# Performance work log

Hardware: AMD Instinct MI355X
Metric: run time of the kernel (lower is better)

The kernel has to match this reference:

```python
import jax, jax.numpy as jnp
import numpy as np

B, DIM, H, W = 8, 384, 64, 64
HEADS = 8
D = DIM // HEADS            # 48, per-head channel dim
DH = D // 2                 # 24
D2 = D // 3 * 2             # 32, conv_up hidden width (ratio=3)


def setup_inputs() -> dict:
    key = jax.random.key(0)
    ks = jax.random.split(key, 12)
    rn = lambda k, s, sc=0.05: jax.random.normal(k, s, dtype=jnp.float32) * sc
    return {
        "x": rn(ks[0], (B, DIM, H, W), 1.0),
        "w_qkv": rn(ks[1], (3 * DIM, DIM)),          # 1x1 conv dim->3dim, no bias
        "w_dw": rn(ks[2], (3 * DIM, 1, 3, 3)),       # depthwise 3x3, groups=3dim
        "temperature": jnp.ones((HEADS, 1, 1), jnp.float32),
        "w_ar": rn(ks[3], (1, D)),                   # conv_attn_right
        "w_vr": rn(ks[4], (DH, D)),                  # conv_v_right
        "w_up1": rn(ks[5], (D2, DH)),                # conv_up[0]
        "b_up1": jnp.zeros((D2,), jnp.float32),
        "ln_g": jnp.ones((D2, HEADS, 1), jnp.float32),   # LayerNorm([D2, 8, 1])
        "ln_b": jnp.zeros((D2, HEADS, 1), jnp.float32),
        "w_up2": rn(ks[6], (D, D2)),                 # conv_up[3]
        "b_up2": jnp.zeros((D,), jnp.float32),
        "w_al": rn(ks[7], (DH, D)),                  # conv_attn_left
        "w_vl": rn(ks[8], (DH, D)),                  # conv_v_left
        "w_proj": rn(ks[9], (DIM, HEADS)),           # project_out: Conv2d(heads, dim, 1)
    }


def reference(x, w_qkv, w_dw, temperature, w_ar, w_vr, w_up1, b_up1,
              ln_g, ln_b, w_up2, b_up2, w_al, w_vl, w_proj):
    b, c, h, w = x.shape
    hw = h * w
    # qkv = dwconv3x3(conv1x1(x)); the torch module computes this identically in
    # both spatial_pool and channel_pool, so compute once.
    qkv = jnp.einsum('oc,bchw->bohw', w_qkv, x)
    qkv = jax.lax.conv_general_dilated(
        qkv, w_dw, window_strides=(1, 1), padding='SAME',
        feature_group_count=3 * c, dimension_numbers=('NCHW', 'OIHW', 'NCHW'))
    q, k, v = jnp.split(qkv, 3, axis=1)
    hsplit = lambda t: t.reshape(b, HEADS, D, hw)        # 'b (head c) h w -> b head c (h w)'
    q, k, v = hsplit(q), hsplit(k), hsplit(v)
    l2n = lambda t: t / jnp.maximum(jnp.linalg.norm(t, axis=-1, keepdims=True), 1e-12)
    # elementwise q*k attention, temperature-scaled, softmax over spatial (hw)
    attn = jax.nn.softmax(l2n(q) * l2n(k) * temperature, axis=-1)   # [b,heads,D,hw]

    # ---- spatial_pool branch (produces channel gate) ----
    input_x = jnp.einsum('od,bhdn->bhon', w_vr, v)                  # [b,heads,DH,hw]
    cmask = jax.nn.softmax(jnp.einsum('od,bhdn->bhon', w_ar, attn), axis=-1)  # [b,heads,1,hw]
    ctx = jnp.einsum('bhin,bhjn->bhji', cmask, input_x)             # [b,heads,DH,1]
    ctx = ctx.transpose(0, 2, 1, 3)                                 # [b,DH,heads,1]
    t = jnp.einsum('op,bphl->bohl', w_up1, ctx) + b_up1[None, :, None, None]  # [b,D2,8,1]
    mu = t.mean(axis=(1, 2, 3), keepdims=True)
    var = t.var(axis=(1, 2, 3), keepdims=True)
    t = (t - mu) / jnp.sqrt(var + 1e-5) * ln_g[None] + ln_b[None]
    t = jax.nn.relu(t)
    t = jnp.einsum('op,bphl->bohl', w_up2, t) + b_up2[None, :, None, None]    # [b,D,8,1]
    # torch .view(b, head*d, 1, 1) on a [b, d, head, 1] tensor: plain reshape
    mask_ch = jax.nn.sigmoid(t).reshape(b, c, 1, 1)
    out_spatial = x * mask_ch

    # ---- channel_pool branch (produces spatial gate) ----
    g_x = jnp.einsum('od,bhdn->bhon', w_al, attn)                   # [b,heads,DH,hw]
    avg_x = jax.nn.softmax(g_x.mean(axis=-1), axis=-1)              # [b,heads,DH]
    theta_x = jnp.einsum('od,bhdn->bhon', w_vl, v)                  # [b,heads,DH,hw]
    mask_sp = jax.nn.sigmoid(jnp.einsum('bho,bhon->bhn', avg_x, theta_x))
    mask_sp = mask_sp.reshape(b, HEADS, h, w)
    mask_sp = jnp.einsum('oh,bhxy->boxy', w_proj, mask_sp)          # project_out
    out_channel = x * mask_sp

    return out_spatial + out_channel
```

## Files before the change

### kernel.cpp

```cpp
#include <hip/hip_runtime.h>
#include <math.h>
#include <stdint.h>

#define B_     8
#define DIM_   384
#define HEADS_ 8
#define D_     48
#define DH_    24
#define D2_    32
#define HW_    4096
#define IMG    64
#define CH3    1152

typedef __attribute__((ext_vector_type(8))) __bf16   bf16x8;
typedef __attribute__((ext_vector_type(4))) float    f32x4;
typedef __attribute__((ext_vector_type(8))) unsigned short u16x8;

__device__ __forceinline__ float b2f(unsigned short h){
  union { uint32_t u; float f; } v; v.u = ((uint32_t)h) << 16; return v.f;
}
__device__ __forceinline__ unsigned short f2b(float f){
  union { float f; uint32_t u; } v; v.f = f;
  uint32_t r = v.u + 0x7fffu + ((v.u >> 16) & 1u);
  return (unsigned short)(r >> 16);
}

__device__ __forceinline__ float wred_sum(float v){
#pragma unroll
  for (int m = 32; m; m >>= 1) v += __shfl_xor(v, m);
  return v;
}
__device__ __forceinline__ float wred_max(float v){
#pragma unroll
  for (int m = 32; m; m >>= 1) v = fmaxf(v, __shfl_xor(v, m));
  return v;
}
__device__ __forceinline__ float wred_min(float v){
#pragma unroll
  for (int m = 32; m; m >>= 1) v = fminf(v, __shfl_xor(v, m));
  return v;
}
template<int OP>
__device__ __forceinline__ float block_red(float v, float* lds){
  if (OP == 0) v = wred_sum(v);
  else if (OP == 1) v = wred_max(v);
  else v = wred_min(v);
  const int lane = threadIdx.x & 63;
  const int wid  = threadIdx.x >> 6;
  __syncthreads();
  if (lane == 0) lds[wid] = v;
  __syncthreads();
  const int nw = blockDim.x >> 6;
  float r = lds[0];
  for (int i = 1; i < nw; ++i){
    float o = lds[i];
    if (OP == 0) r += o; else if (OP == 1) r = fmaxf(r, o); else r = fminf(r, o);
  }
  return r;
}

__device__ __forceinline__ void dwplane16(const unsigned short* __restrict__ plane,
                                          const float* w9, int y, int x0, float* acc16){
#pragma unroll
  for (int j = 0; j < 16; ++j) acc16[j] = 0.f;
#pragma unroll
  for (int dy = -1; dy <= 1; ++dy){
    const int yy = y + dy;
    if ((unsigned)yy >= (unsigned)IMG) continue;
    const unsigned short* rp = plane + yy * IMG;
    u16x8 C0 = *reinterpret_cast<const u16x8*>(rp + x0);
    u16x8 C1 = *reinterpret_cast<const u16x8*>(rp + x0 + 8);
    float rw[18];
    rw[0]  = (x0 > 0)  ? b2f(rp[x0 - 1])  : 0.f;
    rw[17] = (x0 < 48) ? b2f(rp[x0 + 16]) : 0.f;
#pragma unroll
    for (int j = 0; j < 8; ++j){ rw[1+j] = b2f(C0[j]); rw[9+j] = b2f(C1[j]); }
    const float w0 = w9[(dy+1)*3], w1 = w9[(dy+1)*3+1], w2 = w9[(dy+1)*3+2];
#pragma unroll
    for (int j = 0; j < 16; ++j)
      acc16[j] = fmaf(rw[j], w0, fmaf(rw[j+1], w1, fmaf(rw[j+2], w2, acc16[j])));
  }
}

__global__ __launch_bounds__(256)
void k_cvtw(const float* __restrict__ w, unsigned short* __restrict__ wb){
  const int i = (blockIdx.x * 256 + threadIdx.x) * 4;
  float4 v = *reinterpret_cast<const float4*>(w + i);
  wb[i+0] = f2b(v.x); wb[i+1] = f2b(v.y); wb[i+2] = f2b(v.z); wb[i+3] = f2b(v.w);
}

__global__ __launch_bounds__(256)
void k_prep(const float* __restrict__ x, unsigned short* __restrict__ xT){
  __shared__ unsigned short Ts[64][66];
  const int t = threadIdx.x;
  const float* xb = x + ((size_t)blockIdx.z * DIM_ + blockIdx.y * 64) * HW_ + blockIdx.x * 64;
#pragma unroll
  for (int rr = 0; rr < 4; ++rr){
    const int r = (t >> 4) + rr * 16;
    const int c = (t & 15) * 4;
    float4 v = *reinterpret_cast<const float4*>(xb + (size_t)r * HW_ + c);
    Ts[r][c+0] = f2b(v.x); Ts[r][c+1] = f2b(v.y); Ts[r][c+2] = f2b(v.z); Ts[r][c+3] = f2b(v.w);
  }
  __syncthreads();
  const int rn = t >> 2, kc = (t & 3) * 16;
  unsigned short* yb = xT + ((size_t)blockIdx.z * HW_ + blockIdx.x * 64 + rn) * DIM_
                          + blockIdx.y * 64 + kc;
  u16x8 o0, o1;
#pragma unroll
  for (int j = 0; j < 8; ++j){ o0[j] = Ts[kc + j][rn]; o1[j] = Ts[kc + 8 + j][rn]; }
  *reinterpret_cast<u16x8*>(yb)     = o0;
  *reinterpret_cast<u16x8*>(yb + 8) = o1;
}

__global__ __launch_bounds__(256)
void k_gemm(const unsigned short* __restrict__ wb, const unsigned short* __restrict__ xT,
            unsigned short* __restrict__ qkv){
  const int b  = blockIdx.z;
  const int m0 = blockIdx.y * 128;
  const int n0 = blockIdx.x * 128;
  __shared__ unsigned short As[2][128 * 64];
  __shared__ unsigned short Bs[2][128 * 64];
  const int t = threadIdx.x;
  const int lane = t & 63;
  const int fr = lane & 15;
  const int ld = lane >> 4;
  const int w = t >> 6, wr = w >> 1, wc = w & 1;
  f32x4 acc[4][4];
#pragma unroll
  for (int i = 0; i < 4; ++i)
#pragma unroll
    for (int j = 0; j < 4; ++j) acc[i][j] = (f32x4){0.f,0.f,0.f,0.f};

  const unsigned short* Ag = wb + (size_t)m0 * DIM_;
  const unsigned short* Bg = xT + ((size_t)b * HW_ + n0) * DIM_;

  auto stage = [&](int buf, int k0){
#pragma unroll
    for (int i = 0; i < 4; ++i){
      const int q = i * 256 + t;
      const int qb = q & ~63;
      const int r = q >> 3, c = q & 7;
      const int cs = c ^ (r & 7);
      __builtin_amdgcn_global_load_lds(
        (const __attribute__((address_space(1))) void*)(Ag + (size_t)r * DIM_ + k0 + cs * 8),
        (__attribute__((address_space(3))) void*)(&As[buf][qb * 8]), 16, 0, 0);
    }
#pragma unroll
    for (int i = 0; i < 4; ++i){
      const int q = i * 256 + t;
      const int qb = q & ~63;
      const int r = q >> 3, c = q & 7;
      const int cs = c ^ (r & 7);
      __builtin_amdgcn_global_load_lds(
        (const __attribute__((address_space(1))) void*)(Bg + (size_t)r * DIM_ + k0 + cs * 8),
        (__attribute__((address_space(3))) void*)(&Bs[buf][qb * 8]), 16, 0, 0);
    }
  };

  stage(0, 0);
  for (int it = 0; it < 6; ++it){
    const int cur = it & 1;
    if (it < 5){
      stage(cur ^ 1, (it + 1) * 64);
      asm volatile("s_waitcnt vmcnt(8)" ::: "memory");
    } else {
      asm volatile("s_waitcnt vmcnt(0)" ::: "memory");
    }
    __builtin_amdgcn_s_barrier();
    asm volatile("" ::: "memory");
#pragma unroll
    for (int ks = 0; ks < 2; ++ks){
      bf16x8 af[4], bfr[4];
#pragma unroll
      for (int mi = 0; mi < 4; ++mi){
        const int row = wr * 64 + mi * 16 + fr;
        const int cc = (ks * 4 + ld) ^ (row & 7);
        af[mi] = *reinterpret_cast<const bf16x8*>(&As[cur][row * 64 + cc * 8]);
      }
#pragma unroll
      for (int ni = 0; ni < 4; ++ni){
        const int row = wc * 64 + ni * 16 + fr;
        const int cc = (ks * 4 + ld) ^ (row & 7);
        bfr[ni] = *reinterpret_cast<const bf16x8*>(&Bs[cur][row * 64 + cc * 8]);
      }
#pragma unroll
      for (int mi = 0; mi < 4; ++mi)
#pragma unroll
        for (int ni = 0; ni < 4; ++ni)
          acc[mi][ni] = __builtin_amdgcn_mfma_f32_16x16x32_bf16(af[mi], bfr[ni], acc[mi][ni], 0, 0, 0);
    }
    asm volatile("" ::: "memory");
    __builtin_amdgcn_s_barrier();
  }
  unsigned short* yb = qkv + ((size_t)b * CH3 + m0) * HW_ + n0;
#pragma unroll
  for (int mi = 0; mi < 4; ++mi){
    const int rbase = wr * 64 + mi * 16 + (lane >> 4) * 4;
#pragma unroll
    for (int ni = 0; ni < 4; ++ni){
      const int col = wc * 64 + ni * 16 + (lane & 15);
#pragma unroll
      for (int r = 0; r < 4; ++r)
        yb[(size_t)(rbase + r) * HW_ + col] = f2b(acc[mi][ni][r]);
    }
  }
}

__global__ __launch_bounds__(256)
void k_dwqk(unsigned short* __restrict__ qkv, const float* __restrict__ w_dw,
            const float* __restrict__ temperature, const float* __restrict__ w_ar,
            float* __restrict__ prm){
  const int pc = blockIdx.x;
  const int ch = pc % DIM_;
  const int b  = pc / DIM_;
  const int d  = ch % D_;
  const int head = ch / D_;
  unsigned short* qp = qkv + ((size_t)b * CH3 + ch) * HW_;
  unsigned short* kp = qp + (size_t)DIM_ * HW_;
  const int t  = threadIdx.x;
  const int y  = t >> 2;
  const int x0 = (t & 3) * 16;
  float wq9[9], wk9[9];
#pragma unroll
  for (int i = 0; i < 9; ++i){ wq9[i] = w_dw[ch*9+i]; wk9[i] = w_dw[(DIM_+ch)*9+i]; }
  float aq[16], ak[16];
  dwplane16(qp, wq9, y, x0, aq);
  dwplane16(kp, wk9, y, x0, ak);
  unsigned short qs[16], kss[16];
#pragma unroll
  for (int j = 0; j < 16; ++j){ qs[j] = f2b(aq[j]); kss[j] = f2b(ak[j]); }
  __shared__ float lds[8];
  float p[16];
  float sq = 0.f, sk = 0.f, pmx = -3.0e38f, pmn = 3.0e38f;
#pragma unroll
  for (int j = 0; j < 16; ++j){
    const float fq = b2f(qs[j]), fk = b2f(kss[j]);
    sq = fmaf(fq, fq, sq); sk = fmaf(fk, fk, sk);
    p[j] = fq * fk; pmx = fmaxf(pmx, p[j]); pmn = fminf(pmn, p[j]);
  }
  sq  = block_red<0>(sq, lds);
  sk  = block_red<0>(sk, lds);
  pmx = block_red<1>(pmx, lds);
  pmn = block_red<2>(pmn, lds);
  const float nq = fmaxf(sqrtf(sq), 1e-12f);
  const float nk = fmaxf(sqrtf(sk), 1e-12f);
  const float c  = temperature[head] / (nq * nk);
  const float m  = (c >= 0.f) ? c * pmx : c * pmn;
  float se = 0.f;
#pragma unroll
  for (int j = 0; j < 16; ++j) se += expf(fmaf(c, p[j], -m));
  se = block_red<0>(se, lds);
  u16x8 o0, o1;
#pragma unroll
  for (int j = 0; j < 8; ++j){ o0[j] = qs[j]; o1[j] = qs[8+j]; }
  *reinterpret_cast<u16x8*>(qp + (size_t)y * IMG + x0)     = o0;
  *reinterpret_cast<u16x8*>(qp + (size_t)y * IMG + x0 + 8) = o1;
#pragma unroll
  for (int j = 0; j < 8; ++j){ o0[j] = kss[j]; o1[j] = kss[8+j]; }
  *reinterpret_cast<u16x8*>(kp + (size_t)y * IMG + x0)     = o0;
  *reinterpret_cast<u16x8*>(kp + (size_t)y * IMG + x0 + 8) = o1;
  if (t == 0){
    prm[pc*3+0] = c;
    prm[pc*3+1] = m;
    prm[pc*3+2] = w_ar[d] / se;
  }
}

__global__ __launch_bounds__(256)
void k_dwv(unsigned short* __restrict__ qkv, const float* __restrict__ w_dw){
  const int pc = blockIdx.x;
  const int ch = pc % DIM_;
  const int b  = pc / DIM_;
  const int cv = 2*DIM_ + ch;
  unsigned short* plane = qkv + ((size_t)b * CH3 + cv) * HW_;
  const int t  = threadIdx.x;
  const int y  = t >> 2;
  const int x0 = (t & 3) * 16;
  float w9[9];
#pragma unroll
  for (int i = 0; i < 9; ++i) w9[i] = w_dw[cv*9+i];
  float acc16[16];
  dwplane16(plane, w9, y, x0, acc16);
  __syncthreads();
  u16x8 o0, o1;
#pragma unroll
  for (int j = 0; j < 8; ++j){ o0[j] = f2b(acc16[j]); o1[j] = f2b(acc16[8+j]); }
  *reinterpret_cast<u16x8*>(plane + (size_t)y * IMG + x0)     = o0;
  *reinterpret_cast<u16x8*>(plane + (size_t)y * IMG + x0 + 8) = o1;
}

__global__ __launch_bounds__(256)
void k_attn_a(const unsigned short* __restrict__ dqkv, const float* __restrict__ prm,
              float* __restrict__ abuf){
  const int bh   = blockIdx.y;
  const int head = bh & 7, b = bh >> 3;
  const int t = threadIdx.x;
  const int px0 = (blockIdx.x * 256 + t) * 2;
  __shared__ float pc[D_ * 3];
  for (int i = t; i < D_ * 3; i += 256) pc[i] = prm[bh * (D_ * 3) + i];
  __syncthreads();
  const unsigned short* qb = dqkv + ((size_t)b * CH3 + head * D_) * HW_ + px0;
  const unsigned short* kb = qb + (size_t)DIM_ * HW_;
  float a0 = 0.f, a1 = 0.f;
  for (int d = 0; d < D_; ++d){
    const uint32_t qv = *reinterpret_cast<const uint32_t*>(qb + (size_t)d * HW_);
    const uint32_t kv = *reinterpret_cast<const uint32_t*>(kb + (size_t)d * HW_);
    const float cc = pc[d*3], mm = pc[d*3+1], ww = pc[d*3+2];
    const float p0 = b2f((unsigned short)qv) * b2f((unsigned short)kv);
    const float p1 = b2f((unsigned short)(qv >> 16)) * b2f((unsigned short)(kv >> 16));
    a0 = fmaf(ww, expf(fmaf(cc, p0, -mm)), a0);
    a1 = fmaf(ww, expf(fmaf(cc, p1, -mm)), a1);
  }
  float2 o; o.x = a0; o.y = a1;
  *reinterpret_cast<float2*>(abuf + (size_t)bh * HW_ + px0) = o;
}

__global__ __launch_bounds__(256)
void k_cmask(float* __restrict__ abuf){
  const int bh = blockIdx.x;
  float* a = abuf + (size_t)bh * HW_;
  __shared__ float lds[8];
  const int t = threadIdx.x;
  float va[16];
  float mx = -3.0e38f;
#pragma unroll
  for (int i = 0; i < 16; ++i){ va[i] = a[t + i*256]; mx = fmaxf(mx, va[i]); }
  mx = block_red<1>(mx, lds);
  float s = 0.f;
#pragma unroll
  for (int i = 0; i < 16; ++i){ va[i] = expf(va[i]-mx); s += va[i]; }
  s = block_red<0>(s, lds);
  const float inv = 1.f / s;
#pragma unroll
  for (int i = 0; i < 16; ++i) a[t + i*256] = va[i]*inv;
}

__global__ __launch_bounds__(256)
void k_vctx(const unsigned short* __restrict__ dqkv, const float* __restrict__ abuf,
            float* __restrict__ vctx){
  const int bid  = blockIdx.x;
  const int d    = bid % D_;
  const int head = (bid / D_) % HEADS_;
  const int b    = bid / (D_ * HEADS_);
  const unsigned short* vp = dqkv + ((size_t)b * CH3 + 2*DIM_ + head*D_ + d) * HW_;
  const float* cm = abuf + ((size_t)(b * HEADS_ + head)) * HW_;
  __shared__ float lds[8];
  const int t = threadIdx.x;
  float s = 0.f;
  u16x8 v0 = *reinterpret_cast<const u16x8*>(vp + t * 16);
  u16x8 v1 = *reinterpret_cast<const u16x8*>(vp + t * 16 + 8);
#pragma unroll
  for (int j = 0; j < 8; ++j) s = fmaf(cm[t*16 + j],     b2f(v0[j]), s);
#pragma unroll
  for (int j = 0; j < 8; ++j) s = fmaf(cm[t*16 + 8 + j], b2f(v1[j]), s);
  s = block_red<0>(s, lds);
  if (t == 0) vctx[bid] = s;
}

__global__ __launch_bounds__(256)
void k_spmask(const unsigned short* __restrict__ dqkv, const float* __restrict__ w_al,
              const float* __restrict__ w_vl, float* __restrict__ spb){
  const int bh   = blockIdx.y;
  const int head = bh & 7, b = bh >> 3;
  const int t = threadIdx.x;
  const int px0 = (blockIdx.x * 256 + t) * 2;
  __shared__ float u[D_];
  __shared__ float avg[DH_];
  if (t < DH_){
    float s = 0.f;
    for (int d = 0; d < D_; ++d) s += w_al[t*D_ + d];
    avg[t] = s * (1.f/(float)HW_);
  }
  __syncthreads();
  if (t == 0){
    float mx = avg[0];
    for (int o = 1; o < DH_; ++o) mx = fmaxf(mx, avg[o]);
    float s = 0.f;
    for (int o = 0; o < DH_; ++o){ avg[o] = expf(avg[o]-mx); s += avg[o]; }
    const float inv = 1.f/s;
    for (int o = 0; o < DH_; ++o) avg[o] *= inv;
  }
  __syncthreads();
  if (t < D_){
    float s = 0.f;
    for (int o = 0; o < DH_; ++o) s = fmaf(avg[o], w_vl[o*D_ + t], s);
    u[t] = s;
  }
  __syncthreads();
  const unsigned short* vb = dqkv + ((size_t)b * CH3 + 2*DIM_ + head*D_) * HW_ + px0;
  float a0 = 0.f, a1 = 0.f;
  for (int d = 0; d < D_; ++d){
    const uint32_t vv = *reinterpret_cast<const uint32_t*>(vb + (size_t)d * HW_);
    const float ud = u[d];
    a0 = fmaf(ud, b2f((unsigned short)vv), a0);
    a1 = fmaf(ud, b2f((unsigned short)(vv >> 16)), a1);
  }
  float2 o;
  o.x = 1.f/(1.f + expf(-a0));
  o.y = 1.f/(1.f + expf(-a1));
  *reinterpret_cast<float2*>(spb + (size_t)bh * HW_ + px0) = o;
}

__global__ __launch_bounds__(256)
void k_maskch(const float* __restrict__ vctx, const float* __restrict__ w_vr,
              const float* __restrict__ w_up1, const float* __restrict__ b_up1,
              const float* __restrict__ ln_g, const float* __restrict__ ln_b,
              const float* __restrict__ w_up2, const float* __restrict__ b_up2,
              float* __restrict__ mch){
  const int b = blockIdx.x;
  const int t = threadIdx.x;
  __shared__ float vc[HEADS_*D_];
  __shared__ float cx[HEADS_*DH_];
  __shared__ float t1[D2_*HEADS_];
  __shared__ float lds[8];
  for (int i = t; i < HEADS_*D_; i += 256) vc[i] = vctx[b*HEADS_*D_ + i];
  __syncthreads();
  if (t < HEADS_*DH_){
    const int head = t / DH_, o = t % DH_;
    float s = 0.f;
    for (int d = 0; d < D_; ++d) s = fmaf(w_vr[o*D_+d], vc[head*D_+d], s);
    cx[head*DH_+o] = s;
  }
  __syncthreads();
  const int o2 = t >> 3, hh = t & 7;
  float val = b_up1[o2];
  for (int o = 0; o < DH_; ++o) val = fmaf(w_up1[o2*DH_+o], cx[hh*DH_+o], val);
  const float mu  = block_red<0>(val, lds) * (1.f/256.f);
  const float dv  = val - mu;
  const float var = block_red<0>(dv*dv, lds) * (1.f/256.f);
  float yv = dv / sqrtf(var + 1e-5f);
  yv = fmaf(yv, ln_g[t], ln_b[t]);
  yv = fmaxf(yv, 0.f);
  t1[t] = yv;
  __syncthreads();
  for (int idx = t; idx < D_*HEADS_; idx += 256){
    const int d = idx >> 3, head2 = idx & 7;
    float s = b_up2[d];
    for (int o = 0; o < D2_; ++o) s = fmaf(w_up2[d*D2_+o], t1[o*HEADS_+head2], s);
    mch[b*DIM_ + idx] = 1.f/(1.f + expf(-s));
  }
}

__global__ __launch_bounds__(256)
void k_out(const float* __restrict__ x, const float* __restrict__ spb,
           const float* __restrict__ mch, const float* __restrict__ w_proj,
           float* __restrict__ out){
  const int b  = blockIdx.z;
  const int c0 = blockIdx.y * 16;
  const int n  = blockIdx.x * 1024 + threadIdx.x * 4;
  float4 sv[8];
#pragma unroll
  for (int h = 0; h < 8; ++h)
    sv[h] = *reinterpret_cast<const float4*>(spb + ((size_t)(b*8+h))*HW_ + n);
  for (int ci = 0; ci < 16; ++ci){
    const int c = c0 + ci;
    const float g = mch[b*DIM_ + c];
    float4 gv; gv.x = g; gv.y = g; gv.z = g; gv.w = g;
#pragma unroll
    for (int h = 0; h < 8; ++h){
      const float wp = w_proj[c*8+h];
      gv.x = fmaf(wp, sv[h].x, gv.x); gv.y = fmaf(wp, sv[h].y, gv.y);
      gv.z = fmaf(wp, sv[h].z, gv.z); gv.w = fmaf(wp, sv[h].w, gv.w);
    }
    const size_t off = ((size_t)b*DIM_ + c)*HW_ + n;
    float4 xv = *reinterpret_cast<const float4*>(x + off);
    xv.x *= gv.x; xv.y *= gv.y; xv.z *= gv.z; xv.w *= gv.w;
    *reinterpret_cast<float4*>(out + off) = xv;
  }
}

extern "C" void kernel_launch(void* const* d_in, const int* in_sizes, int n_in,
                              void* d_out, int out_size, void* d_ws, size_t ws_size,
                              hipStream_t stream) {
  const float* x      = (const float*)d_in[0];
  const float* w_qkv  = (const float*)d_in[1];
  const float* w_dw   = (const float*)d_in[2];
  const float* temp   = (const float*)d_in[3];
  const float* w_ar   = (const float*)d_in[4];
  const float* w_vr   = (const float*)d_in[5];
  const float* w_up1  = (const float*)d_in[6];
  const float* b_up1  = (const float*)d_in[7];
  const float* ln_g   = (const float*)d_in[8];
  const float* ln_b   = (const float*)d_in[9];
  const float* w_up2  = (const float*)d_in[10];
  const float* b_up2  = (const float*)d_in[11];
  const float* w_al   = (const float*)d_in[12];
  const float* w_vl   = (const float*)d_in[13];
  const float* w_proj = (const float*)d_in[14];
  float* out = (float*)d_out;

  unsigned short* qkvb = (unsigned short*)d_ws;
  unsigned short* xT   = qkvb + (size_t)B_*CH3*HW_;
  unsigned short* wb   = xT + (size_t)B_*HW_*DIM_;
  float* prm  = (float*)(wb + (size_t)CH3*DIM_);
  float* abuf = prm + 3*B_*HEADS_*D_;
  float* vctx = abuf + (size_t)B_*HEADS_*HW_;
  float* spb  = vctx + B_*HEADS_*D_;
  float* mch  = spb + (size_t)B_*HEADS_*HW_;

  k_cvtw<<<dim3((CH3*DIM_)/1024), 256, 0, stream>>>(w_qkv, wb);
  k_prep<<<dim3(HW_/64, DIM_/64, B_), 256, 0, stream>>>(x, xT);
  k_gemm<<<dim3(HW_/128, CH3/128, B_), 256, 0, stream>>>(wb, xT, qkvb);
  k_dwqk<<<dim3(B_*DIM_), 256, 0, stream>>>(qkvb, w_dw, temp, w_ar, prm);
  k_dwv<<<dim3(B_*DIM_), 256, 0, stream>>>(qkvb, w_dw);
  k_attn_a<<<dim3(8, B_*HEADS_), 256, 0, stream>>>(qkvb, prm, abuf);
  k_cmask<<<dim3(B_*HEADS_), 256, 0, stream>>>(abuf);
  k_vctx<<<dim3(B_*HEADS_*D_), 256, 0, stream>>>(qkvb, abuf, vctx);
  k_spmask<<<dim3(8, B_*HEADS_), 256, 0, stream>>>(qkvb, w_al, w_vl, spb);
  k_maskch<<<dim3(B_), 256, 0, stream>>>(vctx, w_vr, w_up1, b_up1, ln_g, ln_b,
                                         w_up2, b_up2, mch);
  k_out<<<dim3(HW_/1024, DIM_/16, B_), 256, 0, stream>>>(x, spb, mch, w_proj, out);
}
```

Measured before the change: 262.5 us.

## Fuse prep kernels, store q*k product, fold V dwconv and softmax into consumers

```diff
diff --git a/kernel.cpp b/kernel.cpp
--- a/kernel.cpp
+++ b/kernel.cpp
@@ -15,6 +15,7 @@
 typedef __attribute__((ext_vector_type(8))) __bf16   bf16x8;
 typedef __attribute__((ext_vector_type(4))) float    f32x4;
 typedef __attribute__((ext_vector_type(8))) unsigned short u16x8;
+typedef __attribute__((ext_vector_type(4))) unsigned short u16x4;
 
 __device__ __forceinline__ float b2f(unsigned short h){
   union { uint32_t u; float f; } v; v.u = ((uint32_t)h) << 16; return v.f;
@@ -82,18 +83,44 @@
   }
 }
 
-__global__ __launch_bounds__(256)
-void k_cvtw(const float* __restrict__ w, unsigned short* __restrict__ wb){
-  const int i = (blockIdx.x * 256 + threadIdx.x) * 4;
-  float4 v = *reinterpret_cast<const float4*>(w + i);
-  wb[i+0] = f2b(v.x); wb[i+1] = f2b(v.y); wb[i+2] = f2b(v.z); wb[i+3] = f2b(v.w);
-}
-
-__global__ __launch_bounds__(256)
-void k_prep(const float* __restrict__ x, unsigned short* __restrict__ xT){
+__device__ __forceinline__ void dwplane4(const unsigned short* __restrict__ plane,
+                                         const float* w9, int y, int x0, float* acc4){
+#pragma unroll
+  for (int j = 0; j < 4; ++j) acc4[j] = 0.f;
+#pragma unroll
+  for (int dy = -1; dy <= 1; ++dy){
+    const int yy = y + dy;
+    if ((unsigned)yy >= (unsigned)IMG) continue;
+    const unsigned short* rp = plane + yy * IMG;
+    u16x4 C = *reinterpret_cast<const u16x4*>(rp + x0);
+    float rw[6];
+    rw[0] = (x0 > 0)  ? b2f(rp[x0 - 1]) : 0.f;
+    rw[5] = (x0 < 60) ? b2f(rp[x0 + 4]) : 0.f;
+#pragma unroll
+    for (int j = 0; j < 4; ++j) rw[1+j] = b2f(C[j]);
+    const float w0 = w9[(dy+1)*3], w1 = w9[(dy+1)*3+1], w2 = w9[(dy+1)*3+2];
+#pragma unroll
+    for (int j = 0; j < 4; ++j)
+      acc4[j] = fmaf(rw[j], w0, fmaf(rw[j+1], w1, fmaf(rw[j+2], w2, acc4[j])));
+  }
+}
+
+__global__ __launch_bounds__(256)
+void k_prep2(const float* __restrict__ x, const float* __restrict__ w,
+             unsigned short* __restrict__ xT, unsigned short* __restrict__ wb){
   __shared__ unsigned short Ts[64][66];
   const int t = threadIdx.x;
-  const float* xb = x + ((size_t)blockIdx.z * DIM_ + blockIdx.y * 64) * HW_ + blockIdx.x * 64;
+  if (blockIdx.x < 432){
+    const int i = (blockIdx.x * 256 + t) * 4;
+    float4 v = *reinterpret_cast<const float4*>(w + i);
+    wb[i+0] = f2b(v.x); wb[i+1] = f2b(v.y); wb[i+2] = f2b(v.z); wb[i+3] = f2b(v.w);
+    return;
+  }
+  const int id = blockIdx.x - 432;
+  const int bz = id / 384;
+  const int r2 = id % 384;
+  const int by = r2 / 64, bx = r2 % 64;
+  const float* xb = x + ((size_t)bz * DIM_ + by * 64) * HW_ + bx * 64;
 #pragma unroll
   for (int rr = 0; rr < 4; ++rr){
     const int r = (t >> 4) + rr * 16;
@@ -103,8 +130,7 @@
   }
   __syncthreads();
   const int rn = t >> 2, kc = (t & 3) * 16;
-  unsigned short* yb = xT + ((size_t)blockIdx.z * HW_ + blockIdx.x * 64 + rn) * DIM_
-                          + blockIdx.y * 64 + kc;
+  unsigned short* yb = xT + ((size_t)bz * HW_ + bx * 64 + rn) * DIM_ + by * 64 + kc;
   u16x8 o0, o1;
 #pragma unroll
   for (int j = 0; j < 8; ++j){ o0[j] = Ts[kc + j][rn]; o1[j] = Ts[kc + 8 + j][rn]; }
@@ -112,7 +138,7 @@
   *reinterpret_cast<u16x8*>(yb + 8) = o1;
 }
 
-__global__ __launch_bounds__(256)
+__global__ __launch_bounds__(512, 4)
 void k_gemm(const unsigned short* __restrict__ wb, const unsigned short* __restrict__ xT,
             unsigned short* __restrict__ qkv){
   const int b  = blockIdx.z;
@@ -124,10 +150,11 @@
   const int lane = t & 63;
   const int fr = lane & 15;
   const int ld = lane >> 4;
-  const int w = t >> 6, wr = w >> 1, wc = w & 1;
-  f32x4 acc[4][4];
-#pragma unroll
-  for (int i = 0; i < 4; ++i)
+  const int w = t >> 6;
+  const int wr = w >> 1, wc = w & 1;
+  f32x4 acc[2][4];
+#pragma unroll
+  for (int i = 0; i < 2; ++i)
 #pragma unroll
     for (int j = 0; j < 4; ++j) acc[i][j] = (f32x4){0.f,0.f,0.f,0.f};
 
@@ -136,8 +163,8 @@
 
   auto stage = [&](int buf, int k0){
 #pragma unroll
-    for (int i = 0; i < 4; ++i){
-      const int q = i * 256 + t;
+    for (int i = 0; i < 2; ++i){
+      const int q = i * 512 + t;
       const int qb = q & ~63;
       const int r = q >> 3, c = q & 7;
       const int cs = c ^ (r & 7);
@@ -146,8 +173,8 @@
         (__attribute__((address_space(3))) void*)(&As[buf][qb * 8]), 16, 0, 0);
     }
 #pragma unroll
-    for (int i = 0; i < 4; ++i){
-      const int q = i * 256 + t;
+    for (int i = 0; i < 2; ++i){
+      const int q = i * 512 + t;
       const int qb = q & ~63;
       const int r = q >> 3, c = q & 7;
       const int cs = c ^ (r & 7);
@@ -162,7 +189,7 @@
     const int cur = it & 1;
     if (it < 5){
       stage(cur ^ 1, (it + 1) * 64);
-      asm volatile("s_waitcnt vmcnt(8)" ::: "memory");
+      asm volatile("s_waitcnt vmcnt(4)" ::: "memory");
     } else {
       asm volatile("s_waitcnt vmcnt(0)" ::: "memory");
     }
@@ -170,10 +197,10 @@
     asm volatile("" ::: "memory");
 #pragma unroll
     for (int ks = 0; ks < 2; ++ks){
-      bf16x8 af[4], bfr[4];
-#pragma unroll
-      for (int mi = 0; mi < 4; ++mi){
-        const int row = wr * 64 + mi * 16 + fr;
+      bf16x8 af[2], bfr[4];
+#pragma unroll
+      for (int mi = 0; mi < 2; ++mi){
+        const int row = wr * 32 + mi * 16 + fr;
         const int cc = (ks * 4 + ld) ^ (row & 7);
         af[mi] = *reinterpret_cast<const bf16x8*>(&As[cur][row * 64 + cc * 8]);
       }
@@ -184,7 +211,7 @@
         bfr[ni] = *reinterpret_cast<const bf16x8*>(&Bs[cur][row * 64 + cc * 8]);
       }
 #pragma unroll
-      for (int mi = 0; mi < 4; ++mi)
+      for (int mi = 0; mi < 2; ++mi)
 #pragma unroll
         for (int ni = 0; ni < 4; ++ni)
           acc[mi][ni] = __builtin_amdgcn_mfma_f32_16x16x32_bf16(af[mi], bfr[ni], acc[mi][ni], 0, 0, 0);
@@ -194,8 +221,8 @@
   }
   unsigned short* yb = qkv + ((size_t)b * CH3 + m0) * HW_ + n0;
 #pragma unroll
-  for (int mi = 0; mi < 4; ++mi){
-    const int rbase = wr * 64 + mi * 16 + (lane >> 4) * 4;
+  for (int mi = 0; mi < 2; ++mi){
+    const int rbase = wr * 32 + mi * 16 + (lane >> 4) * 4;
 #pragma unroll
     for (int ni = 0; ni < 4; ++ni){
       const int col = wc * 64 + ni * 16 + (lane & 15);
@@ -216,7 +243,7 @@
   const int d  = ch % D_;
   const int head = ch / D_;
   unsigned short* qp = qkv + ((size_t)b * CH3 + ch) * HW_;
-  unsigned short* kp = qp + (size_t)DIM_ * HW_;
+  const unsigned short* kp = qp + (size_t)DIM_ * HW_;
   const int t  = threadIdx.x;
   const int y  = t >> 2;
   const int x0 = (t & 3) * 16;
@@ -226,17 +253,18 @@
   float aq[16], ak[16];
   dwplane16(qp, wq9, y, x0, aq);
   dwplane16(kp, wk9, y, x0, ak);
-  unsigned short qs[16], kss[16];
-#pragma unroll
-  for (int j = 0; j < 16; ++j){ qs[j] = f2b(aq[j]); kss[j] = f2b(ak[j]); }
   __shared__ float lds[8];
-  float p[16];
+  float pr[16];
+  unsigned short pb[16];
   float sq = 0.f, sk = 0.f, pmx = -3.0e38f, pmn = 3.0e38f;
 #pragma unroll
   for (int j = 0; j < 16; ++j){
-    const float fq = b2f(qs[j]), fk = b2f(kss[j]);
+    const float fq = b2f(f2b(aq[j]));
+    const float fk = b2f(f2b(ak[j]));
     sq = fmaf(fq, fq, sq); sk = fmaf(fk, fk, sk);
-    p[j] = fq * fk; pmx = fmaxf(pmx, p[j]); pmn = fminf(pmn, p[j]);
+    pb[j] = f2b(fq * fk);
+    pr[j] = b2f(pb[j]);
+    pmx = fmaxf(pmx, pr[j]); pmn = fminf(pmn, pr[j]);
   }
   sq  = block_red<0>(sq, lds);
   sk  = block_red<0>(sk, lds);
@@ -248,45 +276,18 @@
   const float m  = (c >= 0.f) ? c * pmx : c * pmn;
   float se = 0.f;
 #pragma unroll
-  for (int j = 0; j < 16; ++j) se += expf(fmaf(c, p[j], -m));
+  for (int j = 0; j < 16; ++j) se += expf(fmaf(c, pr[j], -m));
   se = block_red<0>(se, lds);
   u16x8 o0, o1;
 #pragma unroll
-  for (int j = 0; j < 8; ++j){ o0[j] = qs[j]; o1[j] = qs[8+j]; }
+  for (int j = 0; j < 8; ++j){ o0[j] = pb[j]; o1[j] = pb[8+j]; }
   *reinterpret_cast<u16x8*>(qp + (size_t)y * IMG + x0)     = o0;
   *reinterpret_cast<u16x8*>(qp + (size_t)y * IMG + x0 + 8) = o1;
-#pragma unroll
-  for (int j = 0; j < 8; ++j){ o0[j] = kss[j]; o1[j] = kss[8+j]; }
-  *reinterpret_cast<u16x8*>(kp + (size_t)y * IMG + x0)     = o0;
-  *reinterpret_cast<u16x8*>(kp + (size_t)y * IMG + x0 + 8) = o1;
   if (t == 0){
     prm[pc*3+0] = c;
     prm[pc*3+1] = m;
     prm[pc*3+2] = w_ar[d] / se;
   }
-}
-
-__global__ __launch_bounds__(256)
-void k_dwv(unsigned short* __restrict__ qkv, const float* __restrict__ w_dw){
-  const int pc = blockIdx.x;
-  const int ch = pc % DIM_;
-  const int b  = pc / DIM_;
-  const int cv = 2*DIM_ + ch;
-  unsigned short* plane = qkv + ((size_t)b * CH3 + cv) * HW_;
-  const int t  = threadIdx.x;
-  const int y  = t >> 2;
-  const int x0 = (t & 3) * 16;
-  float w9[9];
-#pragma unroll
-  for (int i = 0; i < 9; ++i) w9[i] = w_dw[cv*9+i];
-  float acc16[16];
-  dwplane16(plane, w9, y, x0, acc16);
-  __syncthreads();
-  u16x8 o0, o1;
-#pragma unroll
-  for (int j = 0; j < 8; ++j){ o0[j] = f2b(acc16[j]); o1[j] = f2b(acc16[8+j]); }
-  *reinterpret_cast<u16x8*>(plane + (size_t)y * IMG + x0)     = o0;
-  *reinterpret_cast<u16x8*>(plane + (size_t)y * IMG + x0 + 8) = o1;
 }
 
 __global__ __launch_bounds__(256)
@@ -299,78 +300,75 @@
   __shared__ float pc[D_ * 3];
   for (int i = t; i < D_ * 3; i += 256) pc[i] = prm[bh * (D_ * 3) + i];
   __syncthreads();
-  const unsigned short* qb = dqkv + ((size_t)b * CH3 + head * D_) * HW_ + px0;
-  const unsigned short* kb = qb + (size_t)DIM_ * HW_;
+  const unsigned short* pbase = dqkv + ((size_t)b * CH3 + head * D_) * HW_ + px0;
   float a0 = 0.f, a1 = 0.f;
   for (int d = 0; d < D_; ++d){
-    const uint32_t qv = *reinterpret_cast<const uint32_t*>(qb + (size_t)d * HW_);
-    const uint32_t kv = *reinterpret_cast<const uint32_t*>(kb + (size_t)d * HW_);
+    const uint32_t pv = *reinterpret_cast<const uint32_t*>(pbase + (size_t)d * HW_);
     const float cc = pc[d*3], mm = pc[d*3+1], ww = pc[d*3+2];
-    const float p0 = b2f((unsigned short)qv) * b2f((unsigned short)kv);
-    const float p1 = b2f((unsigned short)(qv >> 16)) * b2f((unsigned short)(kv >> 16));
-    a0 = fmaf(ww, expf(fmaf(cc, p0, -mm)), a0);
-    a1 = fmaf(ww, expf(fmaf(cc, p1, -mm)), a1);
+    a0 = fmaf(ww, expf(fmaf(cc, b2f((unsigned short)pv), -mm)), a0);
+    a1 = fmaf(ww, expf(fmaf(cc, b2f((unsigned short)(pv >> 16)), -mm)), a1);
   }
   float2 o; o.x = a0; o.y = a1;
   *reinterpret_cast<float2*>(abuf + (size_t)bh * HW_ + px0) = o;
 }
 
 __global__ __launch_bounds__(256)
-void k_cmask(float* __restrict__ abuf){
-  const int bh = blockIdx.x;
-  float* a = abuf + (size_t)bh * HW_;
-  __shared__ float lds[8];
-  const int t = threadIdx.x;
-  float va[16];
-  float mx = -3.0e38f;
-#pragma unroll
-  for (int i = 0; i < 16; ++i){ va[i] = a[t + i*256]; mx = fmaxf(mx, va[i]); }
-  mx = block_red<1>(mx, lds);
-  float s = 0.f;
-#pragma unroll
-  for (int i = 0; i < 16; ++i){ va[i] = expf(va[i]-mx); s += va[i]; }
-  s = block_red<0>(s, lds);
-  const float inv = 1.f / s;
-#pragma unroll
-  for (int i = 0; i < 16; ++i) a[t + i*256] = va[i]*inv;
-}
-
-__global__ __launch_bounds__(256)
-void k_vctx(const unsigned short* __restrict__ dqkv, const float* __restrict__ abuf,
-            float* __restrict__ vctx){
+void k_vctx(const unsigned short* __restrict__ qkv, const float* __restrict__ w_dw,
+            const float* __restrict__ abuf, float* __restrict__ vctx){
   const int bid  = blockIdx.x;
   const int d    = bid % D_;
   const int head = (bid / D_) % HEADS_;
   const int b    = bid / (D_ * HEADS_);
-  const unsigned short* vp = dqkv + ((size_t)b * CH3 + 2*DIM_ + head*D_ + d) * HW_;
-  const float* cm = abuf + ((size_t)(b * HEADS_ + head)) * HW_;
+  const int cv   = 2*DIM_ + head*D_ + d;
+  const unsigned short* vp = qkv + ((size_t)b * CH3 + cv) * HW_;
+  const float* am = abuf + ((size_t)(b * HEADS_ + head)) * HW_;
+  float w9[9];
+#pragma unroll
+  for (int i = 0; i < 9; ++i) w9[i] = w_dw[cv*9+i];
   __shared__ float lds[8];
-  const int t = threadIdx.x;
+  const int t  = threadIdx.x;
+  const int y  = t >> 2;
+  const int x0 = (t & 3) * 16;
+  float a16[16];
+#pragma unroll
+  for (int i = 0; i < 4; ++i)
+    *reinterpret_cast<float4*>(&a16[i*4]) =
+      *reinterpret_cast<const float4*>(am + t*16 + i*4);
+  float mx = -3.0e38f;
+#pragma unroll
+  for (int j = 0; j < 16; ++j) mx = fmaxf(mx, a16[j]);
+  mx = block_red<1>(mx, lds);
+  float e16[16];
+  float sl = 0.f;
+#pragma unroll
+  for (int j = 0; j < 16; ++j){ e16[j] = expf(a16[j] - mx); sl += e16[j]; }
+  const float S = block_red<0>(sl, lds);
+  const float inv = 1.f / S;
+  float dv16[16];
+  dwplane16(vp, w9, y, x0, dv16);
   float s = 0.f;
-  u16x8 v0 = *reinterpret_cast<const u16x8*>(vp + t * 16);
-  u16x8 v1 = *reinterpret_cast<const u16x8*>(vp + t * 16 + 8);
-#pragma unroll
-  for (int j = 0; j < 8; ++j) s = fmaf(cm[t*16 + j],     b2f(v0[j]), s);
-#pragma unroll
-  for (int j = 0; j < 8; ++j) s = fmaf(cm[t*16 + 8 + j], b2f(v1[j]), s);
+#pragma unroll
+  for (int j = 0; j < 16; ++j) s = fmaf(e16[j] * inv, dv16[j], s);
   s = block_red<0>(s, lds);
   if (t == 0) vctx[bid] = s;
 }
 
 __global__ __launch_bounds__(256)
-void k_spmask(const unsigned short* __restrict__ dqkv, const float* __restrict__ w_al,
-              const float* __restrict__ w_vl, float* __restrict__ spb){
+void k_spmask(const unsigned short* __restrict__ qkv, const float* __restrict__ w_dw,
+              const float* __restrict__ w_al, const float* __restrict__ w_vl,
+              float* __restrict__ spb){
   const int bh   = blockIdx.y;
   const int head = bh & 7, b = bh >> 3;
   const int t = threadIdx.x;
-  const int px0 = (blockIdx.x * 256 + t) * 2;
   __shared__ float u[D_];
   __shared__ float avg[DH_];
+  __shared__ float wdv[D_*9];
   if (t < DH_){
     float s = 0.f;
     for (int d = 0; d < D_; ++d) s += w_al[t*D_ + d];
     avg[t] = s * (1.f/(float)HW_);
   }
+  for (int i = t; i < D_*9; i += 256) wdv[i] = w_dw[(2*DIM_ + head*D_)*9 + i];
   __syncthreads();
   if (t == 0){
     float mx = avg[0];
@@ -387,18 +385,23 @@
     u[t] = s;
   }
   __syncthreads();
-  const unsigned short* vb = dqkv + ((size_t)b * CH3 + 2*DIM_ + head*D_) * HW_ + px0;
-  float a0 = 0.f, a1 = 0.f;
+  const int y  = blockIdx.x * 16 + (t >> 4);
+  const int x0 = (t & 15) * 4;
+  const unsigned short* vb = qkv + ((size_t)b * CH3 + 2*DIM_ + head*D_) * HW_;
+  float acc[4] = {0.f, 0.f, 0.f, 0.f};
   for (int d = 0; d < D_; ++d){
-    const uint32_t vv = *reinterpret_cast<const uint32_t*>(vb + (size_t)d * HW_);
+    float c4[4];
+    dwplane4(vb + (size_t)d * HW_, &wdv[d*9], y, x0, c4);
     const float ud = u[d];
-    a0 = fmaf(ud, b2f((unsigned short)vv), a0);
-    a1 = fmaf(ud, b2f((unsigned short)(vv >> 16)), a1);
-  }
-  float2 o;
-  o.x = 1.f/(1.f + expf(-a0));
-  o.y = 1.f/(1.f + expf(-a1));
-  *reinterpret_cast<float2*>(spb + (size_t)bh * HW_ + px0) = o;
+#pragma unroll
+    for (int j = 0; j < 4; ++j) acc[j] = fmaf(ud, c4[j], acc[j]);
+  }
+  float4 o;
+  o.x = 1.f/(1.f + expf(-acc[0]));
+  o.y = 1.f/(1.f + expf(-acc[1]));
+  o.z = 1.f/(1.f + expf(-acc[2]));
+  o.w = 1.f/(1.f + expf(-acc[3]));
+  *reinterpret_cast<float4*>(spb + (size_t)bh * HW_ + y * IMG + x0) = o;
 }
 
 __global__ __launch_bounds__(256)
@@ -498,15 +501,12 @@
   float* spb  = vctx + B_*HEADS_*D_;
   float* mch  = spb + (size_t)B_*HEADS_*HW_;
 
-  k_cvtw<<<dim3((CH3*DIM_)/1024), 256, 0, stream>>>(w_qkv, wb);
-  k_prep<<<dim3(HW_/64, DIM_/64, B_), 256, 0, stream>>>(x, xT);
-  k_gemm<<<dim3(HW_/128, CH3/128, B_), 256, 0, stream>>>(wb, xT, qkvb);
+  k_prep2<<<dim3(432 + B_*6*64), 256, 0, stream>>>(x, w_qkv, xT, wb);
+  k_gemm<<<dim3(HW_/128, CH3/128, B_), 512, 0, stream>>>(wb, xT, qkvb);
   k_dwqk<<<dim3(B_*DIM_), 256, 0, stream>>>(qkvb, w_dw, temp, w_ar, prm);
-  k_dwv<<<dim3(B_*DIM_), 256, 0, stream>>>(qkvb, w_dw);
   k_attn_a<<<dim3(8, B_*HEADS_), 256, 0, stream>>>(qkvb, prm, abuf);
-  k_cmask<<<dim3(B_*HEADS_), 256, 0, stream>>>(abuf);
-  k_vctx<<<dim3(B_*HEADS_*D_), 256, 0, stream>>>(qkvb, abuf, vctx);
-  k_spmask<<<dim3(8, B_*HEADS_), 256, 0, stream>>>(qkvb, w_al, w_vl, spb);
+  k_vctx<<<dim3(B_*HEADS_*D_), 256, 0, stream>>>(qkvb, w_dw, abuf, vctx);
+  k_spmask<<<dim3(4, B_*HEADS_), 256, 0, stream>>>(qkvb, w_dw, w_al, w_vl, spb);
   k_maskch<<<dim3(B_), 256, 0, stream>>>(vctx, w_vr, w_up1, b_up1, ln_g, ln_b,
                                          w_up2, b_up2, mch);
   k_out<<<dim3(HW_/1024, DIM_/16, B_), 256, 0, stream>>>(x, spb, mch, w_proj, out);
```

Measured after the change: 302.5 us. 1.15x slower.
